# Kernel optimization log

Measured on AMD Instinct MI355X. Metric: run time of the kernel, lower is better.

The kernel has to match this reference:

```python
import math
import jax, jax.numpy as jnp
import numpy as np

EMB = 1024
HEADS = 16
HD = EMB // HEADS  # 64
MAXPOS = 1024
BATCH = 4
SEQ = 1024


def get_rope_cache(dim, max_pos, theta=10000.0):
    # NOTE: faithfully reproduces the (i - 1) quirk of the source (not the standard i)
    i = jnp.arange(dim // 2, dtype=jnp.float32)
    theta_i = theta ** (-2.0 * (i - 1.0) / dim)
    pos = jnp.arange(max_pos, dtype=jnp.float32)[:, None]
    th = pos * theta_i  # [max_pos, dim//2]
    return jnp.stack([jnp.cos(th), jnp.sin(th)], axis=-1)  # [max_pos, dim//2, 2]


def apply_rope(x, rope_cache):
    # x: [B, H, S, hd]. Source casts pairs to float16 before the complex multiply,
    # then the complex32*complex64 product promotes back to float32 -> emulate via
    # an fp16 round-trip on x, with the rotation itself done in fp32.
    B, H, S, hd = x.shape
    rc = rope_cache[:S]  # [S, hd//2, 2]
    xp = x.reshape(B, H, S, hd // 2, 2).astype(jnp.float16).astype(jnp.float32)
    a, b = xp[..., 0], xp[..., 1]
    cos, sin = rc[..., 0], rc[..., 1]
    rot = jnp.stack([a * cos - b * sin, a * sin + b * cos], axis=-1)
    return rot.reshape(B, H, S, hd)


def setup_inputs() -> dict:
    key = jax.random.key(0)
    ks = jax.random.split(key, 5)
    std = math.sqrt(2.0 / (EMB + EMB))
    x = jax.random.normal(ks[0], (BATCH, SEQ, EMB), dtype=jnp.float32)
    padding_mask = jnp.ones((BATCH, SEQ), dtype=jnp.float32)
    Wq = jax.random.normal(ks[1], (EMB, EMB), dtype=jnp.float32) * std
    Wk = jax.random.normal(ks[2], (EMB, EMB), dtype=jnp.float32) * std
    Wv = jax.random.normal(ks[3], (EMB, EMB), dtype=jnp.float32) * std
    Wo = jax.random.normal(ks[4], (EMB, EMB), dtype=jnp.float32) * std
    rope_cache = get_rope_cache(HD, MAXPOS)
    return {"x": x, "padding_mask": padding_mask, "Wq": Wq, "Wk": Wk,
            "Wv": Wv, "Wo": Wo, "rope_cache": rope_cache}


def reference(x, padding_mask, Wq, Wk, Wv, Wo, rope_cache):
    B, S, E = x.shape

    def heads(t):  # [B,S,E] -> [B,H,S,hd]
        return t.reshape(B, S, HEADS, HD).transpose(0, 2, 1, 3)

    q = heads(x @ Wq.T)
    k = heads(x @ Wk.T)
    v = heads(x @ Wv.T)
    q = apply_rope(q, rope_cache)
    k = apply_rope(k, rope_cache)

    scores = jnp.einsum('bhqd,bhkd->bhqk', q, k)  # [B,H,S,S]
    causal = jnp.tril(jnp.ones((S, S), jnp.float32))
    mask = (causal[None, :, :] * padding_mask[:, None, :])[:, None]  # [B,1,S,S]
    scores = jnp.where(mask == 0, jnp.float32(-1e9), scores) / math.sqrt(HD)
    weights = jax.nn.softmax(scores, axis=-1)

    out = jnp.einsum('bhqk,bhkd->bhqd', weights, v)  # [B,H,S,hd]
    # Faithful to source: transpose(-2,-1) then .view(B,S,-1) scrambles head_dim/seq
    out = out.transpose(0, 1, 3, 2).reshape(B, S, E)
    return out @ Wo.T
```

## Files before the change

### kernel.cpp

```cpp
#include <hip/hip_runtime.h>

#define SEQ   1024
#define HEADS 16
#define HD    64
#define BATCH 4
#define EMB   1024

typedef __attribute__((ext_vector_type(8))) short  short8;
typedef __attribute__((ext_vector_type(4))) float  floatx4;

__device__ __forceinline__ unsigned short f2bf(float f) {
    unsigned u = __builtin_bit_cast(unsigned, f);
    u += 0x7FFF + ((u >> 16) & 1);
    return (unsigned short)(u >> 16);
}

__device__ __forceinline__ void g2l16(const void* g, void* l) {
    __builtin_amdgcn_global_load_lds((const __attribute__((address_space(1))) unsigned int*)g,
                                     (__attribute__((address_space(3))) unsigned int*)l,
                                     16, 0, 0);
}

__device__ __forceinline__ short8 ldsfrag(const unsigned short* base, int row, int cq) {
    int ch = cq ^ (row & 7);
    return *(const short8*)(base + row * 64 + ch * 8);
}

__global__ __launch_bounds__(256) void cvt_kernel(
    const float* __restrict__ x,  const float* __restrict__ wq,
    const float* __restrict__ wk, const float* __restrict__ wv,
    const float* __restrict__ wo,
    unsigned short* __restrict__ xb,  unsigned short* __restrict__ wqb,
    unsigned short* __restrict__ wkb, unsigned short* __restrict__ wvb,
    unsigned short* __restrict__ wob) {
    int blk = blockIdx.x;
    const float* src; unsigned short* dst; int rel;
    if      (blk < 4096) { src = x;  dst = xb;  rel = blk; }
    else if (blk < 5120) { src = wq; dst = wqb; rel = blk - 4096; }
    else if (blk < 6144) { src = wk; dst = wkb; rel = blk - 5120; }
    else if (blk < 7168) { src = wv; dst = wvb; rel = blk - 6144; }
    else                 { src = wo; dst = wob; rel = blk - 7168; }
    size_t i = (size_t)rel * 1024 + threadIdx.x * 4;
    float4 v = *(const float4*)(src + i);
    ushort4 o;
    o.x = f2bf(v.x); o.y = f2bf(v.y); o.z = f2bf(v.z); o.w = f2bf(v.w);
    *(ushort4*)(dst + i) = o;
}

template<int MODE, int TM, int TN>
__global__ __launch_bounds__(256) void gemm_m97(
    const unsigned short* __restrict__ A, const unsigned short* __restrict__ W,
    void* __restrict__ out0, void* __restrict__ out1, void* __restrict__ out2,
    const float* __restrict__ rc, int M, int N, int K) {
    constexpr int IM = TM / 32, JN = TN / 32;
    __shared__ unsigned short As[TM * 64];
    __shared__ unsigned short Bs[TN * 64];
    const int tid  = threadIdx.x;
    const int lane = tid & 63;
    const int wid  = tid >> 6;
    const int l15  = lane & 15, quad = lane >> 4;
    const int wm   = (wid & 1) * (TM / 2), wn = (wid >> 1) * (TN / 2);
    const int m0   = blockIdx.y * TM, n0 = blockIdx.x * TN;
    const int boff = tid * 16;

    floatx4 acc[IM][JN] = {};
    const char* Ab = (const char*)A;
    const char* Wb = (const char*)W;
    const size_t rstride = (size_t)K * 2;

    for (int k0 = 0; k0 < K; k0 += 64) {
#pragma unroll
        for (int c = 0; c < TM / 32; c++) {
            int o = c * 4096 + boff;
            int row = o >> 7;
            int sw  = ((o >> 4) & 7) ^ (row & 7);
            g2l16(Ab + (size_t)(m0 + row) * rstride + (size_t)k0 * 2 + sw * 16, (char*)As + o);
        }
#pragma unroll
        for (int c = 0; c < TN / 32; c++) {
            int o = c * 4096 + boff;
            int row = o >> 7;
            int sw  = ((o >> 4) & 7) ^ (row & 7);
            g2l16(Wb + (size_t)(n0 + row) * rstride + (size_t)k0 * 2 + sw * 16, (char*)Bs + o);
        }
        __syncthreads();
#pragma unroll
        for (int ks = 0; ks < 2; ks++) {
            short8 a[IM], b[JN];
#pragma unroll
            for (int i = 0; i < IM; i++) a[i] = ldsfrag(As, wm + i * 16 + l15, ks * 4 + quad);
#pragma unroll
            for (int j = 0; j < JN; j++) b[j] = ldsfrag(Bs, wn + j * 16 + l15, ks * 4 + quad);
#pragma unroll
            for (int i = 0; i < IM; i++)
#pragma unroll
                for (int j = 0; j < JN; j++)
                    acc[i][j] = __builtin_amdgcn_mfma_f32_16x16x32_bf16(a[i], b[j], acc[i][j], 0, 0, 0);
        }
        __syncthreads();
    }

    const int which = n0 >> 10;
#pragma unroll
    for (int i = 0; i < IM; i++) {
#pragma unroll
        for (int r = 0; r < 4; r++) {
            int m = m0 + wm + i * 16 + quad * 4 + r;
            int bb = m >> 10, s = m & 1023;
#pragma unroll
            for (int j = 0; j < JN; j++) {
                int n = n0 + wn + j * 16 + l15;
                float v = acc[i][j][r];
                if (MODE == 0) {
                    ((float*)out0)[(size_t)m * N + n] = v;
                } else {
                    int nr = n & 1023, h = nr >> 6, d = nr & 63;
                    if (which < 2) {
                        float vp = __shfl_xor(v, 1);
                        float2 cs = *(const float2*)&rc[(size_t)s * 64 + (d & ~1)];
                        v = (l15 & 1) ? (vp * cs.y + v * cs.x) : (v * cs.x - vp * cs.y);
                        unsigned short* dst = (which == 0) ? (unsigned short*)out0
                                                           : (unsigned short*)out1;
                        dst[(((size_t)bb * HEADS + h) * SEQ + s) * HD + d] = f2bf(v);
                    } else {
                        ((unsigned short*)out2)[(((size_t)bb * HEADS + h) * HD + d) * SEQ + s] = f2bf(v);
                    }
                }
            }
        }
    }
}

__global__ __launch_bounds__(128) void attn_kernel(
    const unsigned short* __restrict__ Qb, const unsigned short* __restrict__ Kb,
    const unsigned short* __restrict__ VTb, const float* __restrict__ pm,
    unsigned short* __restrict__ Tb) {
    __shared__ unsigned short Ks[64 * 64];
    __shared__ unsigned short Vs[64 * 64];
    __shared__ unsigned short Ps[2][2][16][72];
    __shared__ float pmf[64];
    const int tid  = threadIdx.x;
    const int lane = tid & 63, wid = tid >> 6;
    const int l15  = lane & 15, quad = lane >> 4;
    const int bh   = blockIdx.x, b = bh >> 4;
    const int q0   = (15 - blockIdx.y) * 64;
    const int qw   = q0 + wid * 32;
    const unsigned short* Qh  = Qb  + (size_t)bh * SEQ * HD;
    const unsigned short* Kh  = Kb  + (size_t)bh * SEQ * HD;
    const unsigned short* VTh = VTb + (size_t)bh * HD * SEQ;
    unsigned short*       Th  = Tb  + (size_t)bh * HD * SEQ;
    const float* pmb = pm + b * SEQ;
    const float SCL2 = 0.125f * 1.44269504088896340736f;

    short8 qf[2][2];
#pragma unroll
    for (int u = 0; u < 2; u++) {
        qf[u][0] = *(const short8*)&Qh[(size_t)(qw + u * 16 + l15) * HD + quad * 8];
        qf[u][1] = *(const short8*)&Qh[(size_t)(qw + u * 16 + l15) * HD + 32 + quad * 8];
    }

    floatx4 ot[2][4] = {};
    float l_lane[2] = {0.f, 0.f};
    const int boff = tid * 16;

    for (int kvc = 0; kvc <= q0; kvc += 64) {
        const char* kg = (const char*)(Kh + (size_t)kvc * HD);
        const char* vg = (const char*)(VTh + kvc);
#pragma unroll
        for (int c = 0; c < 4; c++) {
            int o = c * 2048 + boff;
            int row = o >> 7;
            int sw  = ((o >> 4) & 7) ^ (row & 7);
            g2l16(kg + (size_t)row * 128 + sw * 16, (char*)Ks + o);
            g2l16(vg + (size_t)row * (SEQ * 2) + sw * 16, (char*)Vs + o);
        }
        if (tid < 64) pmf[tid] = (pmb[kvc + tid] != 0.f) ? 1.f : 0.f;
        __syncthreads();

        floatx4 sc[2][4];
#pragma unroll
        for (int st = 0; st < 4; st++) {
            short8 ka0 = ldsfrag(Ks, st * 16 + l15, quad);
            short8 ka1 = ldsfrag(Ks, st * 16 + l15, 4 + quad);
#pragma unroll
            for (int u = 0; u < 2; u++) {
                floatx4 z = {0.f, 0.f, 0.f, 0.f};
                z = __builtin_amdgcn_mfma_f32_16x16x32_bf16(ka0, qf[u][0], z, 0, 0, 0);
                z = __builtin_amdgcn_mfma_f32_16x16x32_bf16(ka1, qf[u][1], z, 0, 0, 0);
                sc[u][st] = z;
            }
        }
#pragma unroll
        for (int u = 0; u < 2; u++) {
            const int qbase = qw + u * 16;
            const int qq = qbase + l15;
            const bool diag = (kvc + 63 > qbase);
#pragma unroll
            for (int st = 0; st < 4; st++) {
                float4 pmv = *(const float4*)&pmf[st * 16 + quad * 4];
                int kvbase = kvc + st * 16 + quad * 4;
                ushort4 pk;
#pragma unroll
                for (int r = 0; r < 4; r++) {
                    float e = exp2f(sc[u][st][r] * SCL2) * ((&pmv.x)[r]);
                    if (diag && (kvbase + r > qq)) e = 0.f;
                    l_lane[u] += e;
                    (&pk.x)[r] = f2bf(e);
                }
                *(ushort4*)&Ps[wid][u][l15][st * 16 + quad * 4] = pk;
            }
        }
        asm volatile("s_waitcnt lgkmcnt(0)" ::: "memory");
        short8 pf[2][2];
#pragma unroll
        for (int u = 0; u < 2; u++) {
            pf[u][0] = *(const short8*)&Ps[wid][u][l15][quad * 8];
            pf[u][1] = *(const short8*)&Ps[wid][u][l15][32 + quad * 8];
        }

#pragma unroll
        for (int jt = 0; jt < 4; jt++) {
            short8 v0 = ldsfrag(Vs, jt * 16 + l15, quad);
            short8 v1 = ldsfrag(Vs, jt * 16 + l15, 4 + quad);
#pragma unroll
            for (int u = 0; u < 2; u++) {
                ot[u][jt] = __builtin_amdgcn_mfma_f32_16x16x32_bf16(v0, pf[u][0], ot[u][jt], 0, 0, 0);
                ot[u][jt] = __builtin_amdgcn_mfma_f32_16x16x32_bf16(v1, pf[u][1], ot[u][jt], 0, 0, 0);
            }
        }
        __syncthreads();
    }

#pragma unroll
    for (int u = 0; u < 2; u++) {
        float l = l_lane[u];
        l += __shfl_xor(l, 16);
        l += __shfl_xor(l, 32);
        float inv = 1.0f / l;
        int q = qw + u * 16 + l15;
#pragma unroll
        for (int jt = 0; jt < 4; jt++)
#pragma unroll
            for (int r = 0; r < 4; r++)
                Th[(size_t)(jt * 16 + quad * 4 + r) * SEQ + q] = f2bf(ot[u][jt][r] * inv);
    }
}

extern "C" void kernel_launch(void* const* d_in, const int* in_sizes, int n_in,
                              void* d_out, int out_size, void* d_ws, size_t ws_size,
                              hipStream_t stream) {
    const float* x  = (const float*)d_in[0];
    const float* pm = (const float*)d_in[1];
    const float* Wq = (const float*)d_in[2];
    const float* Wk = (const float*)d_in[3];
    const float* Wv = (const float*)d_in[4];
    const float* Wo = (const float*)d_in[5];
    const float* rc = (const float*)d_in[6];

    char* base = (char*)d_ws;
    unsigned short* xb   = (unsigned short*)(base);
    unsigned short* wqkv = (unsigned short*)(base + (8u  << 20));
    unsigned short* wob  = (unsigned short*)(base + (14u << 20));
    unsigned short* Qb   = (unsigned short*)(base + (16u << 20));
    unsigned short* Kb   = (unsigned short*)(base + (24u << 20));
    unsigned short* VTb  = (unsigned short*)(base + (32u << 20));
    unsigned short* Tb   = (unsigned short*)(base + (40u << 20));

    cvt_kernel<<<8192, 256, 0, stream>>>(x, Wq, Wk, Wv, Wo,
                                         xb, wqkv, wqkv + (1u << 20), wqkv + (2u << 20), wob);
    gemm_m97<1, 128, 128><<<dim3(24, 32), 256, 0, stream>>>(
        xb, wqkv, (void*)Qb, (void*)Kb, (void*)VTb, rc, 4096, 3072, 1024);
    attn_kernel<<<dim3(64, 16), 128, 0, stream>>>(Qb, Kb, VTb, pm, Tb);
    gemm_m97<0, 128, 64><<<dim3(16, 32), 256, 0, stream>>>(
        Tb, wob, d_out, nullptr, nullptr, nullptr, 4096, 1024, 1024);
}
```

Measured before the change: 193.1 us.

## Double-buffer GEMM and attention K/V loads, enlarge attention and output tiles

Both GEMMs now use a two-stage LDS ping-pong with a 32-wide K slice, so the next tile is fetched while the current one is multiplied, and only one barrier is needed per step. The attention kernel moves to 256 threads covering 128 query rows per block and double-buffers the K/V chunks plus the padding-mask slice. The output projection switches to 128x128 tiles. The aim is to hide global-load latency and reuse K/V across more queries. The cost is more LDS per block, possible lower occupancy, and fewer blocks for the output GEMM (256).

Result: slower. 207.6 us (+7.5%).

```diff
diff --git a/kernel.cpp b/kernel.cpp
--- a/kernel.cpp
+++ b/kernel.cpp
@@ -19,11 +19,6 @@
     __builtin_amdgcn_global_load_lds((const __attribute__((address_space(1))) unsigned int*)g,
                                      (__attribute__((address_space(3))) unsigned int*)l,
                                      16, 0, 0);
-}
-
-__device__ __forceinline__ short8 ldsfrag(const unsigned short* base, int row, int cq) {
-    int ch = cq ^ (row & 7);
-    return *(const short8*)(base + row * 64 + ch * 8);
 }
 
 __global__ __launch_bounds__(256) void cvt_kernel(
@@ -48,13 +43,13 @@
 }
 
 template<int MODE, int TM, int TN>
-__global__ __launch_bounds__(256) void gemm_m97(
+__global__ __launch_bounds__(256) void gemm_db(
     const unsigned short* __restrict__ A, const unsigned short* __restrict__ W,
     void* __restrict__ out0, void* __restrict__ out1, void* __restrict__ out2,
     const float* __restrict__ rc, int M, int N, int K) {
     constexpr int IM = TM / 32, JN = TN / 32;
-    __shared__ unsigned short As[TM * 64];
-    __shared__ unsigned short Bs[TN * 64];
+    __shared__ unsigned short As[2][TM * 32];
+    __shared__ unsigned short Bs[2][TN * 32];
     const int tid  = threadIdx.x;
     const int lane = tid & 63;
     const int wid  = tid >> 6;
@@ -68,37 +63,52 @@
     const char* Wb = (const char*)W;
     const size_t rstride = (size_t)K * 2;
 
-    for (int k0 = 0; k0 < K; k0 += 64) {
-#pragma unroll
-        for (int c = 0; c < TM / 32; c++) {
+    auto stage = [&](int bsel, int k0) {
+#pragma unroll
+        for (int c = 0; c < TM / 64; c++) {
             int o = c * 4096 + boff;
-            int row = o >> 7;
-            int sw  = ((o >> 4) & 7) ^ (row & 7);
-            g2l16(Ab + (size_t)(m0 + row) * rstride + (size_t)k0 * 2 + sw * 16, (char*)As + o);
-        }
-#pragma unroll
-        for (int c = 0; c < TN / 32; c++) {
+            int row = o >> 6;
+            int sw  = ((o >> 4) & 3) ^ (row & 3);
+            g2l16(Ab + (size_t)(m0 + row) * rstride + (size_t)k0 * 2 + sw * 16,
+                  (char*)As[bsel] + o);
+        }
+#pragma unroll
+        for (int c = 0; c < TN / 64; c++) {
             int o = c * 4096 + boff;
-            int row = o >> 7;
-            int sw  = ((o >> 4) & 7) ^ (row & 7);
-            g2l16(Wb + (size_t)(n0 + row) * rstride + (size_t)k0 * 2 + sw * 16, (char*)Bs + o);
-        }
+            int row = o >> 6;
+            int sw  = ((o >> 4) & 3) ^ (row & 3);
+            g2l16(Wb + (size_t)(n0 + row) * rstride + (size_t)k0 * 2 + sw * 16,
+                  (char*)Bs[bsel] + o);
+        }
+    };
+    auto compute = [&](int bsel) {
+        short8 a[IM], b[JN];
+#pragma unroll
+        for (int i = 0; i < IM; i++) {
+            int r = wm + i * 16 + l15;
+            a[i] = *(const short8*)(As[bsel] + r * 32 + (quad ^ (r & 3)) * 8);
+        }
+#pragma unroll
+        for (int j = 0; j < JN; j++) {
+            int r = wn + j * 16 + l15;
+            b[j] = *(const short8*)(Bs[bsel] + r * 32 + (quad ^ (r & 3)) * 8);
+        }
+#pragma unroll
+        for (int i = 0; i < IM; i++)
+#pragma unroll
+            for (int j = 0; j < JN; j++)
+                acc[i][j] = __builtin_amdgcn_mfma_f32_16x16x32_bf16(a[i], b[j], acc[i][j], 0, 0, 0);
+    };
+
+    stage(0, 0);
+    __syncthreads();
+    const int NIT = K / 32;
+    for (int it = 1; it < NIT; ++it) {
+        stage(it & 1, it * 32);
+        compute((it - 1) & 1);
         __syncthreads();
-#pragma unroll
-        for (int ks = 0; ks < 2; ks++) {
-            short8 a[IM], b[JN];
-#pragma unroll
-            for (int i = 0; i < IM; i++) a[i] = ldsfrag(As, wm + i * 16 + l15, ks * 4 + quad);
-#pragma unroll
-            for (int j = 0; j < JN; j++) b[j] = ldsfrag(Bs, wn + j * 16 + l15, ks * 4 + quad);
-#pragma unroll
-            for (int i = 0; i < IM; i++)
-#pragma unroll
-                for (int j = 0; j < JN; j++)
-                    acc[i][j] = __builtin_amdgcn_mfma_f32_16x16x32_bf16(a[i], b[j], acc[i][j], 0, 0, 0);
-        }
-        __syncthreads();
-    }
+    }
+    compute((NIT - 1) & 1);
 
     const int which = n0 >> 10;
 #pragma unroll
@@ -131,19 +141,19 @@
     }
 }
 
-__global__ __launch_bounds__(128) void attn_kernel(
+__global__ __launch_bounds__(256) void attn_kernel(
     const unsigned short* __restrict__ Qb, const unsigned short* __restrict__ Kb,
     const unsigned short* __restrict__ VTb, const float* __restrict__ pm,
     unsigned short* __restrict__ Tb) {
-    __shared__ unsigned short Ks[64 * 64];
-    __shared__ unsigned short Vs[64 * 64];
-    __shared__ unsigned short Ps[2][2][16][72];
-    __shared__ float pmf[64];
+    __shared__ unsigned short Ks[2][64 * 64];
+    __shared__ unsigned short Vs[2][64 * 64];
+    __shared__ unsigned short Ps[4][2][16][72];
+    __shared__ float pmf[2][64];
     const int tid  = threadIdx.x;
     const int lane = tid & 63, wid = tid >> 6;
     const int l15  = lane & 15, quad = lane >> 4;
     const int bh   = blockIdx.x, b = bh >> 4;
-    const int q0   = (15 - blockIdx.y) * 64;
+    const int q0   = (7 - blockIdx.y) * 128;
     const int qw   = q0 + wid * 32;
     const unsigned short* Qh  = Qb  + (size_t)bh * SEQ * HD;
     const unsigned short* Kh  = Kb  + (size_t)bh * SEQ * HD;
@@ -151,6 +161,7 @@
     unsigned short*       Th  = Tb  + (size_t)bh * HD * SEQ;
     const float* pmb = pm + b * SEQ;
     const float SCL2 = 0.125f * 1.44269504088896340736f;
+    const int boff = tid * 16;
 
     short8 qf[2][2];
 #pragma unroll
@@ -161,27 +172,30 @@
 
     floatx4 ot[2][4] = {};
     float l_lane[2] = {0.f, 0.f};
-    const int boff = tid * 16;
-
-    for (int kvc = 0; kvc <= q0; kvc += 64) {
+
+    auto stageKV = [&](int bsel, int kvc) {
         const char* kg = (const char*)(Kh + (size_t)kvc * HD);
         const char* vg = (const char*)(VTh + kvc);
 #pragma unroll
-        for (int c = 0; c < 4; c++) {
-            int o = c * 2048 + boff;
+        for (int c = 0; c < 2; c++) {
+            int o = c * 4096 + boff;
             int row = o >> 7;
             int sw  = ((o >> 4) & 7) ^ (row & 7);
-            g2l16(kg + (size_t)row * 128 + sw * 16, (char*)Ks + o);
-            g2l16(vg + (size_t)row * (SEQ * 2) + sw * 16, (char*)Vs + o);
-        }
-        if (tid < 64) pmf[tid] = (pmb[kvc + tid] != 0.f) ? 1.f : 0.f;
-        __syncthreads();
-
+            g2l16(kg + (size_t)row * 128 + sw * 16, (char*)Ks[bsel] + o);
+            g2l16(vg + (size_t)row * (SEQ * 2) + sw * 16, (char*)Vs[bsel] + o);
+        }
+        if (tid < 64) pmf[bsel][tid] = (pmb[kvc + tid] != 0.f) ? 1.f : 0.f;
+    };
+
+    auto compute_chunk = [&](int bsel, int kvc) {
+        const unsigned short* Kc = Ks[bsel];
+        const unsigned short* Vc = Vs[bsel];
         floatx4 sc[2][4];
 #pragma unroll
         for (int st = 0; st < 4; st++) {
-            short8 ka0 = ldsfrag(Ks, st * 16 + l15, quad);
-            short8 ka1 = ldsfrag(Ks, st * 16 + l15, 4 + quad);
+            int r = st * 16 + l15;
+            short8 ka0 = *(const short8*)(Kc + r * 64 + ((quad ^ (r & 7)) * 8));
+            short8 ka1 = *(const short8*)(Kc + r * 64 + (((4 + quad) ^ (r & 7)) * 8));
 #pragma unroll
             for (int u = 0; u < 2; u++) {
                 floatx4 z = {0.f, 0.f, 0.f, 0.f};
@@ -197,7 +211,7 @@
             const bool diag = (kvc + 63 > qbase);
 #pragma unroll
             for (int st = 0; st < 4; st++) {
-                float4 pmv = *(const float4*)&pmf[st * 16 + quad * 4];
+                float4 pmv = *(const float4*)&pmf[bsel][st * 16 + quad * 4];
                 int kvbase = kvc + st * 16 + quad * 4;
                 ushort4 pk;
 #pragma unroll
@@ -217,19 +231,28 @@
             pf[u][0] = *(const short8*)&Ps[wid][u][l15][quad * 8];
             pf[u][1] = *(const short8*)&Ps[wid][u][l15][32 + quad * 8];
         }
-
 #pragma unroll
         for (int jt = 0; jt < 4; jt++) {
-            short8 v0 = ldsfrag(Vs, jt * 16 + l15, quad);
-            short8 v1 = ldsfrag(Vs, jt * 16 + l15, 4 + quad);
+            int r = jt * 16 + l15;
+            short8 v0 = *(const short8*)(Vc + r * 64 + ((quad ^ (r & 7)) * 8));
+            short8 v1 = *(const short8*)(Vc + r * 64 + (((4 + quad) ^ (r & 7)) * 8));
 #pragma unroll
             for (int u = 0; u < 2; u++) {
                 ot[u][jt] = __builtin_amdgcn_mfma_f32_16x16x32_bf16(v0, pf[u][0], ot[u][jt], 0, 0, 0);
                 ot[u][jt] = __builtin_amdgcn_mfma_f32_16x16x32_bf16(v1, pf[u][1], ot[u][jt], 0, 0, 0);
             }
         }
+    };
+
+    const int nch = q0 / 64 + 2;
+    stageKV(0, 0);
+    __syncthreads();
+    for (int ic = 1; ic < nch; ++ic) {
+        stageKV(ic & 1, ic * 64);
+        compute_chunk((ic - 1) & 1, (ic - 1) * 64);
         __syncthreads();
     }
+    compute_chunk((nch - 1) & 1, (nch - 1) * 64);
 
 #pragma unroll
     for (int u = 0; u < 2; u++) {
@@ -268,9 +291,9 @@
 
     cvt_kernel<<<8192, 256, 0, stream>>>(x, Wq, Wk, Wv, Wo,
                                          xb, wqkv, wqkv + (1u << 20), wqkv + (2u << 20), wob);
-    gemm_m97<1, 128, 128><<<dim3(24, 32), 256, 0, stream>>>(
+    gemm_db<1, 128, 128><<<dim3(24, 32), 256, 0, stream>>>(
         xb, wqkv, (void*)Qb, (void*)Kb, (void*)VTb, rc, 4096, 3072, 1024);
-    attn_kernel<<<dim3(64, 16), 128, 0, stream>>>(Qb, Kb, VTb, pm, Tb);
-    gemm_m97<0, 128, 64><<<dim3(16, 32), 256, 0, stream>>>(
+    attn_kernel<<<dim3(64, 8), 256, 0, stream>>>(Qb, Kb, VTb, pm, Tb);
+    gemm_db<0, 128, 128><<<dim3(8, 32), 256, 0, stream>>>(
         Tb, wob, d_out, nullptr, nullptr, nullptr, 4096, 1024, 1024);
 }
```
